# Performance work log

Hardware: AMD Instinct MI355X
Metric: run time of the kernel (lower is better)

Reference implementation:

```python
import jax, jax.numpy as jnp
import numpy as np

ITER = 18  # prop_time


def _conv3x3(x, w, b):
    # NCHW conv, stride 1, pad 1 (conv_offset_aff)
    y = jax.lax.conv_general_dilated(x, w, window_strides=(1, 1),
                                     padding=((1, 1), (1, 1)),
                                     dimension_numbers=('NCHW', 'OIHW', 'NCHW'))
    return y + b[None, :, None, None]


def _bilinear(img, py, px):
    # img: [H,W]; py/px: [9,H,W] fractional sample coords; zero outside bounds
    H, W = img.shape
    y0 = jnp.floor(py)
    x0 = jnp.floor(px)
    ty = py - y0
    tx = px - x0

    def gather(yf, xf):
        valid = (yf >= 0) & (yf <= H - 1) & (xf >= 0) & (xf <= W - 1)
        yc = jnp.clip(yf, 0, H - 1).astype(jnp.int32)
        xc = jnp.clip(xf, 0, W - 1).astype(jnp.int32)
        return jnp.where(valid, img[yc, xc], 0.0)

    v00 = gather(y0, x0)
    v01 = gather(y0, x0 + 1)
    v10 = gather(y0 + 1, x0)
    v11 = gather(y0 + 1, x0 + 1)
    return (1 - ty) * ((1 - tx) * v00 + tx * v01) + ty * ((1 - tx) * v10 + tx * v11)


def _deform_conv(feat, offset, mask, w9, bias):
    # modulated deformable 3x3 conv, 1 channel, stride 1, pad 1, dil 1
    # offset: [B,18,H,W] in (dy,dx) pairs per kernel tap (torchvision layout)
    B, _, H, W = feat.shape
    off = offset.reshape(B, 9, 2, H, W)
    ky = (jnp.arange(9) // 3 - 1).astype(feat.dtype)  # kernel row offsets
    kx = (jnp.arange(9) % 3 - 1).astype(feat.dtype)   # kernel col offsets
    ys = jnp.arange(H, dtype=feat.dtype)[:, None]
    xs = jnp.arange(W, dtype=feat.dtype)[None, :]
    py = ys[None, None] + ky[None, :, None, None] + off[:, :, 0]  # [B,9,H,W]
    px = xs[None, None] + kx[None, :, None, None] + off[:, :, 1]
    sampled = jax.vmap(_bilinear)(feat[:, 0], py, px)  # [B,9,H,W]
    out = jnp.einsum('bkhw,bkhw,k->bhw', sampled, mask, w9) + bias[0]
    return out[:, None]  # [B,1,H,W]


def _forward(feat_init, guidance, confidence, feat_fix, conv_w, conv_b, w, b):
    conf = jnp.sign(feat_fix) * jax.nn.sigmoid(confidence)
    oa = _conv3x3(guidance, conv_w, conv_b)            # [B,27,H,W]
    offset1 = oa[:, :18].astype(jnp.float16)           # .half() in torch
    aff1 = jax.nn.softmax(oa[:, 18:], axis=1).astype(jnp.float16)
    off_f = offset1.astype(jnp.float32)                # .float() in loop
    aff_f = aff1.astype(jnp.float32)
    w9 = w.reshape(9)

    def step(fr, _):
        fr = (1 - conf) * _deform_conv(fr, off_f, aff_f, w9, b) + conf * feat_fix
        return fr, fr

    pred, list_feat = jax.lax.scan(step, feat_init.astype(jnp.float32), None, length=ITER)
    return pred, list_feat, offset1, aff1


def setup_inputs() -> dict:
    key = jax.random.key(0)
    ks = jax.random.split(key, 6)
    B, H, W = 2, 352, 1216
    feat_init = jax.random.normal(ks[0], (B, 1, H, W), jnp.float32)
    guidance = jax.random.normal(ks[1], (B, 9, H, W), jnp.float32)
    confidence = jax.random.normal(ks[2], (B, 1, H, W), jnp.float32)
    feat_fix = jax.random.normal(ks[3], (B, 1, H, W), jnp.float32)
    # conv_offset_aff params (zero-init in source; small random for a non-trivial baseline)
    conv_w = jax.random.normal(ks[4], (27, 9, 3, 3), jnp.float32) * 0.05
    conv_b = jax.random.normal(ks[5], (27,), jnp.float32) * 0.01
    w = jnp.ones((1, 1, 3, 3), jnp.float32)   # fixed deform-conv weight
    b = jnp.zeros((1,), jnp.float32)          # fixed deform-conv bias
    return {'feat_init': feat_init, 'guidance': guidance, 'confidence': confidence,
            'feat_fix': feat_fix, 'conv_w': conv_w, 'conv_b': conv_b, 'w': w, 'b': b}


def reference(feat_init, guidance, confidence, feat_fix, conv_w, conv_b, w, b):
    return _forward(feat_init, guidance, confidence, feat_fix, conv_w, conv_b, w, b)
```

## Files before the change

kernel.cpp:

```cpp
#include <hip/hip_runtime.h>
#include <hip/hip_fp16.h>

#define HH 352
#define WW 1216
#define HW (HH*WW)
#define NPIX (2*HW)
#define NITER 18
#define PACK_BYTES ((size_t)NPIX * 64)

#define SEGW 256
#define NSEGC ((WW + SEGW - 1) / SEGW)
#define AROW_B 208
#define A_BYTES (256 * AROW_B)
#define B_OFF A_BYTES
#define LDS_BYTES (A_BYTES + 32 * AROW_B)
#define OAROW_B 152

#define SEG 256
#define XHALO 6
#define YHALO 4
#define PROWS 4
#define TROWS (PROWS + 9)
#define TCOLS (SEG + 2*XHALO)
#define NSEG ((WW + SEG - 1) / SEG)

typedef __attribute__((ext_vector_type(8))) short short8;
typedef __attribute__((ext_vector_type(4))) float f32x4;

__device__ __forceinline__ unsigned short f2bf(float f) {
    unsigned u = __float_as_uint(f);
    unsigned r = (u + 0x7fffu + ((u >> 16) & 1u)) >> 16;
    return (unsigned short)r;
}

__global__ __launch_bounds__(256) void conv_mfma_kernel(
    const float* __restrict__ g,
    const float* __restrict__ cw,
    const float* __restrict__ cb,
    const float* __restrict__ confidence,
    const float* __restrict__ feat_fix,
    float* __restrict__ out_off,
    float* __restrict__ out_aff,
    uint4* __restrict__ packed)
{
    __shared__ char lds[LDS_BYTES];

    const int tid = threadIdx.x;
    const int bid = blockIdx.x;
    const int seg = bid % NSEGC;
    const int y   = (bid / NSEGC) % HH;
    const int b   = bid / (NSEGC * HH);
    const int xs  = seg * SEGW;
    const int x   = xs + tid;

    for (int i = tid; i < 32 * 48; i += 256) {
        int n = i / 48;
        int kp = i - n * 48;
        unsigned v = 0;
        if (n < 27) {
            const float* wrow = cw + n * 81;
            int k0 = kp * 2;
            unsigned short h0 = (k0 < 81) ? f2bf(wrow[k0]) : (unsigned short)0;
            unsigned short h1 = (k0 + 1 < 81) ? f2bf(wrow[k0 + 1]) : (unsigned short)0;
            v = (unsigned)h0 | ((unsigned)h1 << 16);
        }
        *(unsigned*)(lds + B_OFF + n * AROW_B + kp * 4) = v;
    }

    {
        const float* gb = g + (size_t)b * 9 * HW;
        unsigned au[48];
#pragma unroll
        for (int j = 0; j < 48; ++j) au[j] = 0;
#pragma unroll
        for (int ci = 0; ci < 9; ++ci)
#pragma unroll
            for (int ty = 0; ty < 3; ++ty) {
                const int row = y + ty - 1;
                const bool vr = ((unsigned)row < HH);
                const float* rp = gb + (size_t)ci * HW + (size_t)(vr ? row : 0) * WW;
                const int cx = xs + tid - 1;
                float L = (vr && (unsigned)cx < WW) ? rp[cx] : 0.f;
                float M = (vr && (unsigned)(cx + 1) < WW) ? rp[cx + 1] : 0.f;
                float R = (vr && (unsigned)(cx + 2) < WW) ? rp[cx + 2] : 0.f;
                const int k = ci * 9 + ty * 3;
                au[(k) >> 1]     |= ((unsigned)f2bf(L)) << (((k) & 1) * 16);
                au[(k + 1) >> 1] |= ((unsigned)f2bf(M)) << (((k + 1) & 1) * 16);
                au[(k + 2) >> 1] |= ((unsigned)f2bf(R)) << (((k + 2) & 1) * 16);
            }
        char* arow = lds + tid * AROW_B;
#pragma unroll
        for (int j = 0; j < 12; ++j)
            *(uint4*)(arow + 16 * j) =
                make_uint4(au[4 * j], au[4 * j + 1], au[4 * j + 2], au[4 * j + 3]);
    }
    __syncthreads();

    const int w = tid >> 6, l = tid & 63;
    const int lrow = l & 15;
    const int lk = (l >> 4) * 8;
    f32x4 acc[4][2];
#pragma unroll
    for (int mt = 0; mt < 4; ++mt)
#pragma unroll
        for (int nt = 0; nt < 2; ++nt)
            acc[mt][nt] = (f32x4){0.f, 0.f, 0.f, 0.f};

#pragma unroll
    for (int kk = 0; kk < 3; ++kk) {
        const int ko = kk * 32 + lk;
        short8 bb0 = *(const short8*)(lds + B_OFF + lrow * AROW_B + ko * 2);
        short8 bb1 = *(const short8*)(lds + B_OFF + (lrow + 16) * AROW_B + ko * 2);
#pragma unroll
        for (int mt = 0; mt < 4; ++mt) {
            short8 aa = *(const short8*)(lds + (w * 64 + mt * 16 + lrow) * AROW_B + ko * 2);
            acc[mt][0] = __builtin_amdgcn_mfma_f32_16x16x32_bf16(aa, bb0, acc[mt][0], 0, 0, 0);
            acc[mt][1] = __builtin_amdgcn_mfma_f32_16x16x32_bf16(aa, bb1, acc[mt][1], 0, 0, 0);
        }
    }
    __syncthreads();

#pragma unroll
    for (int mt = 0; mt < 4; ++mt)
#pragma unroll
        for (int nt = 0; nt < 2; ++nt)
#pragma unroll
            for (int reg = 0; reg < 4; ++reg) {
                int px = w * 64 + mt * 16 + (l >> 4) * 4 + reg;
                int ch = nt * 16 + lrow;
                *(float*)(lds + px * OAROW_B + ch * 4) = acc[mt][nt][reg];
            }
    __syncthreads();

    if (x >= WW) return;
    const int r = y * WW + x;
    const int p = b * HW + r;

    float oa[27];
    {
        const char* orow = lds + tid * OAROW_B;
#pragma unroll
        for (int j = 0; j < 13; ++j) {
            float2 v = *(const float2*)(orow + 8 * j);
            oa[2 * j] = v.x;
            if (2 * j + 1 < 27) oa[2 * j + 1] = v.y;
        }
        oa[26] = *(const float*)(orow + 26 * 4);
#pragma unroll
        for (int c = 0; c < 27; ++c) oa[c] += cb[c];
    }

    __half h[28];
#pragma unroll
    for (int c = 0; c < 18; ++c) h[c] = __float2half(oa[c]);

    float m = oa[18];
#pragma unroll
    for (int c = 19; c < 27; ++c) m = fmaxf(m, oa[c]);
    float e[9], s = 0.f;
#pragma unroll
    for (int k = 0; k < 9; ++k) { e[k] = expf(oa[18 + k] - m); s += e[k]; }
    float inv = 1.f / s;
#pragma unroll
    for (int k = 0; k < 9; ++k) h[18 + k] = __float2half(e[k] * inv);
    h[27] = __float2half(0.f);

#pragma unroll
    for (int c = 0; c < 18; ++c)
        out_off[(size_t)b * 18 * HW + (size_t)c * HW + r] = __half2float(h[c]);
#pragma unroll
    for (int k = 0; k < 9; ++k)
        out_aff[(size_t)b * 9 * HW + (size_t)k * HW + r] = __half2float(h[18 + k]);

    if (packed) {
        float cf = confidence[p];
        float ff = feat_fix[p];
        float sg = (ff > 0.f) ? 1.f : ((ff < 0.f) ? -1.f : 0.f);
        float conf = sg / (1.f + expf(-cf));

        unsigned uu[16];
#pragma unroll
        for (int i = 0; i < 14; ++i)
            uu[i] = (unsigned)__half_as_ushort(h[2 * i]) |
                    ((unsigned)__half_as_ushort(h[2 * i + 1]) << 16);
        uu[14] = __float_as_uint(1.f - conf);
        uu[15] = __float_as_uint(conf * ff);

        uint4* dst = packed + (size_t)p * 4;
        dst[0] = make_uint4(uu[0], uu[1], uu[2], uu[3]);
        dst[1] = make_uint4(uu[4], uu[5], uu[6], uu[7]);
        dst[2] = make_uint4(uu[8], uu[9], uu[10], uu[11]);
        dst[3] = make_uint4(uu[12], uu[13], uu[14], uu[15]);
    }
}

__global__ __launch_bounds__(256) void prop4_kernel(
    const float* __restrict__ src,
    float* __restrict__ dst,
    const uint4* __restrict__ packed,
    const float* __restrict__ w9,
    const float* __restrict__ biasp,
    float* __restrict__ out_pred)
{
    __shared__ float tile[TROWS * TCOLS];

    const int xs = blockIdx.x * SEG;
    const int y0 = blockIdx.y * PROWS;
    const int b  = blockIdx.z;
    const float* sf = src + (size_t)b * HW;

    for (int i = threadIdx.x; i < TROWS * TCOLS; i += 256) {
        int rr = i / TCOLS;
        int cc = i - rr * TCOLS;
        int gy = y0 - YHALO + rr;
        int gx = xs - XHALO + cc;
        float v = 0.f;
        if ((unsigned)gy < HH && (unsigned)gx < WW)
            v = sf[(size_t)gy * WW + gx];
        tile[i] = v;
    }
    __syncthreads();

    const int x = xs + threadIdx.x;
    if (x >= WW) return;
    const float bias = biasp[0];

#pragma unroll 1
    for (int ty = 0; ty < PROWS; ++ty) {
        const int y = y0 + ty;
        const int r = y * WW + x;
        const int p = b * HW + r;

        const uint4* pk = packed + (size_t)p * 4;
        uint4 q0 = pk[0], q1 = pk[1], q2 = pk[2], q3 = pk[3];
        unsigned uu[14] = {q0.x, q0.y, q0.z, q0.w, q1.x, q1.y, q1.z, q1.w,
                           q2.x, q2.y, q2.z, q2.w, q3.x, q3.y};
        float hv[27];
#pragma unroll
        for (int i = 0; i < 13; ++i) {
            hv[2 * i]     = __half2float(__ushort_as_half((unsigned short)(uu[i] & 0xffff)));
            hv[2 * i + 1] = __half2float(__ushort_as_half((unsigned short)(uu[i] >> 16)));
        }
        hv[26] = __half2float(__ushort_as_half((unsigned short)(uu[13] & 0xffff)));
        float cm1 = __uint_as_float(q3.z);
        float cff = __uint_as_float(q3.w);

        float acc = 0.f;
#pragma unroll
        for (int k = 0; k < 9; ++k) {
            float py = (float)y + (float)(k / 3 - 1) + hv[2 * k];
            float px = (float)x + (float)(k % 3 - 1) + hv[2 * k + 1];
            float y0f = floorf(py), x0f = floorf(px);
            float tyf = py - y0f, txf = px - x0f;
            int iy = (int)y0f, ix = (int)x0f;

            int ly = iy - y0 + YHALO;
            int lx = ix - xs + XHALO;
            float v00, v01, v10, v11;
            if ((unsigned)ly < (TROWS - 1) && (unsigned)lx < (TCOLS - 1)) {
                const float* t0 = &tile[ly * TCOLS + lx];
                v00 = t0[0];     v01 = t0[1];
                v10 = t0[TCOLS]; v11 = t0[TCOLS + 1];
            } else {
                bool vy0 = ((unsigned)iy < HH), vy1 = ((unsigned)(iy + 1) < HH);
                bool vx0 = ((unsigned)ix < WW), vx1 = ((unsigned)(ix + 1) < WW);
                v00 = (vy0 && vx0) ? sf[(size_t)iy * WW + ix] : 0.f;
                v01 = (vy0 && vx1) ? sf[(size_t)iy * WW + ix + 1] : 0.f;
                v10 = (vy1 && vx0) ? sf[(size_t)(iy + 1) * WW + ix] : 0.f;
                v11 = (vy1 && vx1) ? sf[(size_t)(iy + 1) * WW + ix + 1] : 0.f;
            }
            float top = (1.f - txf) * v00 + txf * v01;
            float bot = (1.f - txf) * v10 + txf * v11;
            float sv = (1.f - tyf) * top + tyf * bot;
            acc = fmaf(sv * hv[18 + k], w9[k], acc);
        }
        float dc = acc + bias;
        float fr = fmaf(cm1, dc, cff);

        dst[p] = fr;
        if (out_pred) out_pred[p] = fr;
    }
}

__global__ __launch_bounds__(256) void prop_kernel(
    const float* __restrict__ src,
    float* __restrict__ dst,
    const float* __restrict__ off,
    const float* __restrict__ aff,
    const float* __restrict__ confidence,
    const float* __restrict__ feat_fix,
    const float* __restrict__ w9,
    const float* __restrict__ biasp,
    float* __restrict__ out_pred)
{
    int p = blockIdx.x * 256 + threadIdx.x;
    if (p >= NPIX) return;
    int b = p / HW;
    int r = p - b * HW;
    int y = r / WW;
    int x = r - y * WW;

    const float* offb = off + (size_t)b * 18 * HW + r;
    const float* affb = aff + (size_t)b * 9 * HW + r;
    const float* sf = src + (size_t)b * HW;

    float acc = 0.f;
#pragma unroll
    for (int k = 0; k < 9; ++k) {
        float dy = offb[(size_t)(2 * k) * HW];
        float dx = offb[(size_t)(2 * k + 1) * HW];
        float af = affb[(size_t)k * HW];
        float py = (float)y + (float)(k / 3 - 1) + dy;
        float px = (float)x + (float)(k % 3 - 1) + dx;
        float y0f = floorf(py), x0f = floorf(px);
        float ty = py - y0f, tx = px - x0f;
        int iy = (int)y0f, ix = (int)x0f;
        bool vy0 = ((unsigned)iy < HH), vy1 = ((unsigned)(iy + 1) < HH);
        bool vx0 = ((unsigned)ix < WW), vx1 = ((unsigned)(ix + 1) < WW);
        float v00 = (vy0 && vx0) ? sf[(size_t)iy * WW + ix] : 0.f;
        float v01 = (vy0 && vx1) ? sf[(size_t)iy * WW + ix + 1] : 0.f;
        float v10 = (vy1 && vx0) ? sf[(size_t)(iy + 1) * WW + ix] : 0.f;
        float v11 = (vy1 && vx1) ? sf[(size_t)(iy + 1) * WW + ix + 1] : 0.f;
        float top = (1.f - tx) * v00 + tx * v01;
        float bot = (1.f - tx) * v10 + tx * v11;
        float sv = (1.f - ty) * top + ty * bot;
        acc = fmaf(sv * af, w9[k], acc);
    }
    float dc = acc + biasp[0];

    float cf = confidence[p];
    float ffv = feat_fix[p];
    float sg = (ffv > 0.f) ? 1.f : ((ffv < 0.f) ? -1.f : 0.f);
    float conf = sg / (1.f + expf(-cf));
    float fr = (1.f - conf) * dc + conf * ffv;

    dst[p] = fr;
    if (out_pred) out_pred[p] = fr;
}

extern "C" void kernel_launch(void* const* d_in, const int* in_sizes, int n_in,
                              void* d_out, int out_size, void* d_ws, size_t ws_size,
                              hipStream_t stream) {
    const float* feat_init  = (const float*)d_in[0];
    const float* guidance   = (const float*)d_in[1];
    const float* confidence = (const float*)d_in[2];
    const float* feat_fix   = (const float*)d_in[3];
    const float* conv_w     = (const float*)d_in[4];
    const float* conv_b     = (const float*)d_in[5];
    const float* w          = (const float*)d_in[6];
    const float* bias       = (const float*)d_in[7];

    float* outf = (float*)d_out;
    float* out_pred = outf;
    float* out_list = outf + (size_t)NPIX;
    float* out_off  = outf + (size_t)19 * NPIX;
    float* out_aff  = outf + (size_t)37 * NPIX;

    bool use_pack = (ws_size >= PACK_BYTES);
    uint4* packed = use_pack ? (uint4*)d_ws : nullptr;

    conv_mfma_kernel<<<NSEGC * HH * 2, 256, 0, stream>>>(
        guidance, conv_w, conv_b, confidence, feat_fix,
        out_off, out_aff, packed);

    dim3 pgrid(NSEG, HH / PROWS, 2);
    int blocks = (NPIX + 255) / 256;
    const float* src = feat_init;
    for (int it = 0; it < NITER; ++it) {
        float* dstf = out_list + (size_t)it * NPIX;
        float* predp = (it == NITER - 1) ? out_pred : nullptr;
        if (use_pack) {
            prop4_kernel<<<pgrid, 256, 0, stream>>>(
                src, dstf, packed, w, bias, predp);
        } else {
            prop_kernel<<<blocks, 256, 0, stream>>>(
                src, dstf, out_off, out_aff, confidence, feat_fix, w, bias, predp);
        }
        src = dstf;
    }
}
```

Before: 372.8 us.

## Fold deform weights and bias into packed affinities; shrink conv segment width

```diff
diff --git a/kernel.cpp b/kernel.cpp
--- a/kernel.cpp
+++ b/kernel.cpp
@@ -8,10 +8,10 @@
 #define NITER 18
 #define PACK_BYTES ((size_t)NPIX * 64)
 
-#define SEGW 256
+#define SEGW 192
 #define NSEGC ((WW + SEGW - 1) / SEGW)
 #define AROW_B 208
-#define A_BYTES (256 * AROW_B)
+#define A_BYTES (SEGW * AROW_B)
 #define B_OFF A_BYTES
 #define LDS_BYTES (A_BYTES + 32 * AROW_B)
 #define OAROW_B 152
@@ -39,6 +39,8 @@
     const float* __restrict__ cb,
     const float* __restrict__ confidence,
     const float* __restrict__ feat_fix,
+    const float* __restrict__ w9,
+    const float* __restrict__ biasp,
     float* __restrict__ out_off,
     float* __restrict__ out_aff,
     uint4* __restrict__ packed)
@@ -67,7 +69,7 @@
         *(unsigned*)(lds + B_OFF + n * AROW_B + kp * 4) = v;
     }
 
-    {
+    if (tid < SEGW) {
         const float* gb = g + (size_t)b * 9 * HW;
         unsigned au[48];
 #pragma unroll
@@ -79,7 +81,7 @@
                 const int row = y + ty - 1;
                 const bool vr = ((unsigned)row < HH);
                 const float* rp = gb + (size_t)ci * HW + (size_t)(vr ? row : 0) * WW;
-                const int cx = xs + tid - 1;
+                const int cx = x - 1;
                 float L = (vr && (unsigned)cx < WW) ? rp[cx] : 0.f;
                 float M = (vr && (unsigned)(cx + 1) < WW) ? rp[cx + 1] : 0.f;
                 float R = (vr && (unsigned)(cx + 2) < WW) ? rp[cx + 2] : 0.f;
@@ -99,9 +101,9 @@
     const int w = tid >> 6, l = tid & 63;
     const int lrow = l & 15;
     const int lk = (l >> 4) * 8;
-    f32x4 acc[4][2];
-#pragma unroll
-    for (int mt = 0; mt < 4; ++mt)
+    f32x4 acc[3][2];
+#pragma unroll
+    for (int mt = 0; mt < 3; ++mt)
 #pragma unroll
         for (int nt = 0; nt < 2; ++nt)
             acc[mt][nt] = (f32x4){0.f, 0.f, 0.f, 0.f};
@@ -112,8 +114,8 @@
         short8 bb0 = *(const short8*)(lds + B_OFF + lrow * AROW_B + ko * 2);
         short8 bb1 = *(const short8*)(lds + B_OFF + (lrow + 16) * AROW_B + ko * 2);
 #pragma unroll
-        for (int mt = 0; mt < 4; ++mt) {
-            short8 aa = *(const short8*)(lds + (w * 64 + mt * 16 + lrow) * AROW_B + ko * 2);
+        for (int mt = 0; mt < 3; ++mt) {
+            short8 aa = *(const short8*)(lds + (w * 48 + mt * 16 + lrow) * AROW_B + ko * 2);
             acc[mt][0] = __builtin_amdgcn_mfma_f32_16x16x32_bf16(aa, bb0, acc[mt][0], 0, 0, 0);
             acc[mt][1] = __builtin_amdgcn_mfma_f32_16x16x32_bf16(aa, bb1, acc[mt][1], 0, 0, 0);
         }
@@ -121,18 +123,18 @@
     __syncthreads();
 
 #pragma unroll
-    for (int mt = 0; mt < 4; ++mt)
+    for (int mt = 0; mt < 3; ++mt)
 #pragma unroll
         for (int nt = 0; nt < 2; ++nt)
 #pragma unroll
             for (int reg = 0; reg < 4; ++reg) {
-                int px = w * 64 + mt * 16 + (l >> 4) * 4 + reg;
+                int px = w * 48 + mt * 16 + (l >> 4) * 4 + reg;
                 int ch = nt * 16 + lrow;
                 *(float*)(lds + px * OAROW_B + ch * 4) = acc[mt][nt][reg];
             }
     __syncthreads();
 
-    if (x >= WW) return;
+    if (tid >= SEGW || x >= WW) return;
     const int r = y * WW + x;
     const int p = b * HW + r;
 
@@ -150,7 +152,7 @@
         for (int c = 0; c < 27; ++c) oa[c] += cb[c];
     }
 
-    __half h[28];
+    __half h[27];
 #pragma unroll
     for (int c = 0; c < 18; ++c) h[c] = __float2half(oa[c]);
 
@@ -163,7 +165,6 @@
     float inv = 1.f / s;
 #pragma unroll
     for (int k = 0; k < 9; ++k) h[18 + k] = __float2half(e[k] * inv);
-    h[27] = __float2half(0.f);
 
 #pragma unroll
     for (int c = 0; c < 18; ++c)
@@ -177,14 +178,26 @@
         float ff = feat_fix[p];
         float sg = (ff > 0.f) ? 1.f : ((ff < 0.f) ? -1.f : 0.f);
         float conf = sg / (1.f + expf(-cf));
+        float cm1 = 1.f - conf;
+        float bias = biasp[0];
+
+        __half hw[9];
+#pragma unroll
+        for (int k = 0; k < 9; ++k)
+            hw[k] = __float2half(__half2float(h[18 + k]) * w9[k]);
 
         unsigned uu[16];
 #pragma unroll
-        for (int i = 0; i < 14; ++i)
+        for (int i = 0; i < 9; ++i)
             uu[i] = (unsigned)__half_as_ushort(h[2 * i]) |
                     ((unsigned)__half_as_ushort(h[2 * i + 1]) << 16);
-        uu[14] = __float_as_uint(1.f - conf);
-        uu[15] = __float_as_uint(conf * ff);
+#pragma unroll
+        for (int j = 0; j < 4; ++j)
+            uu[9 + j] = (unsigned)__half_as_ushort(hw[2 * j]) |
+                        ((unsigned)__half_as_ushort(hw[2 * j + 1]) << 16);
+        uu[13] = (unsigned)__half_as_ushort(hw[8]);
+        uu[14] = __float_as_uint(cm1);
+        uu[15] = __float_as_uint(fmaf(cm1, bias, conf * ff));
 
         uint4* dst = packed + (size_t)p * 4;
         dst[0] = make_uint4(uu[0], uu[1], uu[2], uu[3]);
@@ -198,8 +211,6 @@
     const float* __restrict__ src,
     float* __restrict__ dst,
     const uint4* __restrict__ packed,
-    const float* __restrict__ w9,
-    const float* __restrict__ biasp,
     float* __restrict__ out_pred)
 {
     __shared__ float tile[TROWS * TCOLS];
@@ -223,13 +234,11 @@
 
     const int x = xs + threadIdx.x;
     if (x >= WW) return;
-    const float bias = biasp[0];
 
 #pragma unroll 1
     for (int ty = 0; ty < PROWS; ++ty) {
         const int y = y0 + ty;
-        const int r = y * WW + x;
-        const int p = b * HW + r;
+        const int p = b * HW + y * WW + x;
 
         const uint4* pk = packed + (size_t)p * 4;
         uint4 q0 = pk[0], q1 = pk[1], q2 = pk[2], q3 = pk[3];
@@ -242,16 +251,16 @@
             hv[2 * i + 1] = __half2float(__ushort_as_half((unsigned short)(uu[i] >> 16)));
         }
         hv[26] = __half2float(__ushort_as_half((unsigned short)(uu[13] & 0xffff)));
-        float cm1 = __uint_as_float(q3.z);
-        float cff = __uint_as_float(q3.w);
+        const float cm1 = __uint_as_float(q3.z);
+        const float cff = __uint_as_float(q3.w);
 
         float acc = 0.f;
 #pragma unroll
         for (int k = 0; k < 9; ++k) {
-            float py = (float)y + (float)(k / 3 - 1) + hv[2 * k];
-            float px = (float)x + (float)(k % 3 - 1) + hv[2 * k + 1];
-            float y0f = floorf(py), x0f = floorf(px);
-            float tyf = py - y0f, txf = px - x0f;
+            float py  = (float)(y + k / 3 - 1) + hv[2 * k];
+            float pxx = (float)(x + k % 3 - 1) + hv[2 * k + 1];
+            float y0f = floorf(py), x0f = floorf(pxx);
+            float tyf = py - y0f, txf = pxx - x0f;
             int iy = (int)y0f, ix = (int)x0f;
 
             int ly = iy - y0 + YHALO;
@@ -269,13 +278,12 @@
                 v10 = (vy1 && vx0) ? sf[(size_t)(iy + 1) * WW + ix] : 0.f;
                 v11 = (vy1 && vx1) ? sf[(size_t)(iy + 1) * WW + ix + 1] : 0.f;
             }
-            float top = (1.f - txf) * v00 + txf * v01;
-            float bot = (1.f - txf) * v10 + txf * v11;
-            float sv = (1.f - tyf) * top + tyf * bot;
-            acc = fmaf(sv * hv[18 + k], w9[k], acc);
-        }
-        float dc = acc + bias;
-        float fr = fmaf(cm1, dc, cff);
+            float top = fmaf(txf, v01 - v00, v00);
+            float bot = fmaf(txf, v11 - v10, v10);
+            float sv  = fmaf(tyf, bot - top, top);
+            acc = fmaf(sv, hv[18 + k], acc);
+        }
+        float fr = fmaf(cm1, acc, cff);
 
         dst[p] = fr;
         if (out_pred) out_pred[p] = fr;
@@ -360,7 +368,7 @@
     uint4* packed = use_pack ? (uint4*)d_ws : nullptr;
 
     conv_mfma_kernel<<<NSEGC * HH * 2, 256, 0, stream>>>(
-        guidance, conv_w, conv_b, confidence, feat_fix,
+        guidance, conv_w, conv_b, confidence, feat_fix, w, bias,
         out_off, out_aff, packed);
 
     dim3 pgrid(NSEG, HH / PROWS, 2);
@@ -370,8 +378,7 @@
         float* dstf = out_list + (size_t)it * NPIX;
         float* predp = (it == NITER - 1) ? out_pred : nullptr;
         if (use_pack) {
-            prop4_kernel<<<pgrid, 256, 0, stream>>>(
-                src, dstf, packed, w, bias, predp);
+            prop4_kernel<<<pgrid, 256, 0, stream>>>(src, dstf, packed, predp);
         } else {
             prop_kernel<<<blocks, 256, 0, stream>>>(
                 src, dstf, out_off, out_aff, confidence, feat_fix, w, bias, predp);
```

Measured after the change: 359.7 us (median of 3 runs). 3.5% less time.
